# Optimization experiments

Measured on AMD Instinct MI355X. Metric: run time of the kernel, lower is better.

## Reference

```python
import jax, jax.numpy as jnp
import numpy as np

IN_DIM = 512
HID = 1024
E = 16
TOPK = 2


def setup_inputs() -> dict:
    key = jax.random.key(0)
    ks = jax.random.split(key, 8)
    s = 0.02
    x = jax.random.normal(ks[0], (4, 2048, IN_DIM), dtype=jnp.float32)
    Wr = jax.random.normal(ks[1], (IN_DIM, E), dtype=jnp.float32) * s
    br = jnp.zeros((E,), dtype=jnp.float32)
    W1 = jax.random.normal(ks[2], (E, IN_DIM, HID), dtype=jnp.float32) * s
    b1 = jnp.zeros((E, HID), dtype=jnp.float32)
    W2 = jax.random.normal(ks[3], (E, HID, IN_DIM), dtype=jnp.float32) * s
    b2 = jnp.zeros((E, IN_DIM), dtype=jnp.float32)
    return {"x": x, "Wr": Wr, "br": br, "W1": W1, "b1": b1, "W2": W2, "b2": b2}


def reference(x, Wr, br, W1, b1, W2, b2):
    token_shape = x.shape[:-1]
    xf = x.reshape(-1, x.shape[-1])            # [T, D]
    T = xf.shape[0]

    # router (temperature = 1.0)
    logits = xf @ Wr + br                       # [T, E]
    probs = jax.nn.softmax(logits, axis=-1)
    topk_w, topk_idx = jax.lax.top_k(probs, TOPK)           # [T, K]
    topk_w = topk_w / jnp.maximum(topk_w.sum(-1, keepdims=True), 1e-9)

    # combine weights: [T, E], zero where not routed
    combine = jnp.zeros((T, E), dtype=xf.dtype).at[
        jnp.arange(T)[:, None], topk_idx].add(topk_w)

    # per-expert MLP (exact GELU, as torch nn.GELU default), weighted combine
    y = jnp.zeros_like(xf)
    for e in range(E):
        h = jax.nn.gelu(xf @ W1[e] + b1[e], approximate=False)  # [T, H]
        o = h @ W2[e] + b2[e]                                   # [T, D]
        y = y + combine[:, e:e + 1] * o

    # residual (in_dim == out_dim)
    y = xf + y
    return y.reshape(*token_shape, IN_DIM)
```

## Files before the change

kernel.cpp:

```cpp
#include <hip/hip_runtime.h>
#include <hip/hip_bf16.h>
#include <math.h>

#define IN_DIM 512
#define HID    1024
#define NE     16
#define T_TOK  8192
#define NPAIR  (T_TOK*2)

typedef __attribute__((ext_vector_type(8))) short bf16x8;
typedef __attribute__((ext_vector_type(8))) unsigned short ushort8;
typedef __attribute__((ext_vector_type(4))) float f32x4;

__device__ __forceinline__ unsigned short f2b(float f){
  unsigned u = __float_as_uint(f);
  u += 0x7FFF + ((u >> 16) & 1);
  return (unsigned short)(u >> 16);
}
__device__ __forceinline__ float b2f(unsigned short u){
  return __uint_as_float(((unsigned)u) << 16);
}

__device__ __forceinline__ void barrier_lds_only(){
  asm volatile("s_waitcnt lgkmcnt(0)" ::: "memory");
  __builtin_amdgcn_s_barrier();
}

__global__ __launch_bounds__(256) void fused_head(
    const float* __restrict__ x, const float* __restrict__ Wr, const float* __restrict__ br,
    unsigned short* __restrict__ xb, int* __restrict__ eid, float* __restrict__ pw,
    const float* __restrict__ W1, unsigned short* __restrict__ O1,
    const float* __restrict__ W2, unsigned short* __restrict__ O2)
{
  __shared__ float tile[64][65];
  const int b = blockIdx.x;
  const int tid = threadIdx.x;

  if (b < 2048){
    int wid = tid >> 6, lane = tid & 63;
    int t = b*4 + wid;
    const float4* xr4 = (const float4*)(x + (size_t)t*IN_DIM);
    ushort4*      xb4 = (ushort4*)(xb + (size_t)t*IN_DIM);

    float acc[NE];
    #pragma unroll
    for (int i=0;i<NE;i++) acc[i]=0.f;

    #pragma unroll
    for (int j=0;j<2;j++){
      int f = j*64 + lane;
      float4 v = xr4[f];
      ushort4 o; o.x=f2b(v.x); o.y=f2b(v.y); o.z=f2b(v.z); o.w=f2b(v.w);
      xb4[f] = o;
      const float4* wr4 = (const float4*)(Wr + (size_t)(f*4)*NE);
      const float* vv = (const float*)&v;
      #pragma unroll
      for (int rr=0; rr<4; rr++){
        float xv = vv[rr];
        #pragma unroll
        for (int q=0;q<4;q++){
          float4 w = wr4[rr*4+q];
          acc[q*4+0] += xv*w.x; acc[q*4+1] += xv*w.y;
          acc[q*4+2] += xv*w.z; acc[q*4+3] += xv*w.w;
        }
      }
    }
    #pragma unroll
    for (int off=32; off>=1; off>>=1){
      #pragma unroll
      for (int i=0;i<NE;i++) acc[i] += __shfl_xor(acc[i], off, 64);
    }
    if (lane==0){
      #pragma unroll
      for (int i=0;i<NE;i++) acc[i] += br[i];
      int e0=0; float l0=acc[0];
      #pragma unroll
      for (int i=1;i<NE;i++) if (acc[i] > l0){ l0=acc[i]; e0=i; }
      int e1=-1; float l1=-3.0e38f;
      #pragma unroll
      for (int i=0;i<NE;i++) if (i!=e0 && acc[i] > l1){ l1=acc[i]; e1=i; }
      float w0 = 1.f/(1.f + __expf(l1 - l0));
      float w1 = 1.f - w0;
      pw[t*2+0] = w0; pw[t*2+1] = w1;
      eid[t*2+0] = e0; eid[t*2+1] = e1;
    }
    return;
  }

  const float* src; unsigned short* dst; int M, N, m0, n0;
  const int bb = b - 2048;
  if (bb < 2048){
    M = IN_DIM; N = HID;
    int e = bb >> 7, r = bb & 127;
    n0 = (r & 15)*64; m0 = (r >> 4)*64;
    src = W1 + (size_t)e*M*N; dst = O1 + (size_t)e*M*N;
  } else {
    int b2 = bb - 2048; M = HID; N = IN_DIM;
    int e = b2 >> 7, r = b2 & 127;
    n0 = (r & 7)*64; m0 = (r >> 3)*64;
    src = W2 + (size_t)e*M*N; dst = O2 + (size_t)e*M*N;
  }
  const int lr = tid >> 4, lc = (tid & 15)*4;
  #pragma unroll
  for (int i=0;i<4;i++)
    *(float4*)&tile[lr + i*16][lc] = *(const float4*)&src[(size_t)(m0 + lr + i*16)*N + n0 + lc];
  __syncthreads();
  const int nr = tid >> 3, mc = (tid & 7)*8;
  #pragma unroll
  for (int p=0;p<2;p++){
    int n = nr + p*32;
    ushort8 o;
    #pragma unroll
    for (int j=0;j<8;j++) o[j] = f2b(tile[mc+j][n]);
    *(ushort8*)&dst[(size_t)(n0 + n)*M + m0 + mc] = o;
  }
}

__global__ __launch_bounds__(1024) void bucket_kernel(const int* __restrict__ eid,
                                                      int* __restrict__ cnt,
                                                      int* __restrict__ bucket){
  int e = blockIdx.x;
  __shared__ int lbase;
  if (threadIdx.x == 0) lbase = 0;
  __syncthreads();
  int lane = threadIdx.x & 63, wid = threadIdx.x >> 6;
  int* be = bucket + e*T_TOK;
  for (int c = wid*64; c < NPAIR; c += 1024){
    int p = c + lane;
    bool ok = (eid[p] == e);
    unsigned long long m = __ballot(ok);
    int rank = __popcll(m & ((1ull << lane) - 1ull));
    int count = __popcll(m);
    int base = 0;
    if (lane == 0) base = atomicAdd(&lbase, count);
    base = __shfl(base, 0, 64);
    if (ok) be[base + rank] = p;
  }
  __syncthreads();
  if (threadIdx.x == 0) cnt[e] = lbase;
}

template<int KDIM, int NDIM, bool FIRST>
__global__ __launch_bounds__(256) void moe_gemm(
    const unsigned short* __restrict__ A,
    const unsigned short* __restrict__ Bm,
    const float* __restrict__ bias,
    const int* __restrict__ cnt,
    const int* __restrict__ bucket,
    const float* __restrict__ pw,
    unsigned short* __restrict__ hb,
    unsigned short* __restrict__ opb)
{
  constexpr int NS  = KDIM / 32;
  constexpr int NBT = NDIM / 128;

  int ntiles = 0;
  #pragma unroll
  for (int j=0;j<NE;j++) ntiles += ((cnt[j]+63)>>6)*NBT;

  __shared__ unsigned short As[2*64*32];
  __shared__ unsigned short Bs[2*128*32];

  int tid = threadIdx.x;
  int lane = tid & 63, wid = tid >> 6;
  int wm = (wid>>1)*32, wn = (wid&1)*64;
  int lr0 = tid >> 2;
  int c   = tid & 3;
  int sc  = (c ^ ((lr0 >> 1) & 3)) * 8;
  int wA  = lr0*32 + sc;
  int fr = lane & 15, fb = lane >> 4;
  int pf8 = (fb ^ ((fr >> 1) & 3)) * 8;
  int fq = (lane>>4)*4;

  const int t0 = (blockIdx.x & 7)*(gridDim.x >> 3) + (blockIdx.x >> 3);
  for (int t = t0; t < ntiles; t += gridDim.x){
    int e=0, tloc=0, ebase=0, ce=0, itl=1;
    {
      int cum=0, crow=0;
      #pragma unroll
      for (int j=0;j<NE;j++){
        int cj = cnt[j];
        int it = (cj+63)>>6;
        int tj = it * NBT;
        bool in = (t >= cum) & (t < cum+tj);
        if (in){ e=j; tloc=t-cum; ebase=crow; ce=cj; itl=it; }
        cum += tj; crow += cj;
      }
    }
    int i0 = (tloc % itl) * 64;
    int n0 = (tloc / itl) * 128;

    const int* buck = bucket + e*T_TOK;
    int posA = i0 + lr0;
    int arow;
    if (FIRST){
      int pair = (posA < ce) ? buck[posA] : buck[i0];
      arow = pair >> 1;
    } else {
      arow = ebase + posA;
      if (arow > NPAIR-1) arow = NPAIR-1;
    }
    const unsigned short* Ag = A + (size_t)arow*KDIM + c*8;
    const unsigned short* Bg = Bm + (size_t)e*NDIM*KDIM + (size_t)(n0 + lr0)*KDIM + c*8;

    f32x4 acc[2][4];
    #pragma unroll
    for (int a=0;a<2;a++)
      #pragma unroll
      for (int b2=0;b2<4;b2++)
        #pragma unroll
        for (int j=0;j<4;j++) acc[a][b2][j] = 0.f;

    float4 ar, br0, br1;
    ar  = *(const float4*)(Ag);
    br0 = *(const float4*)(Bg);
    br1 = *(const float4*)(Bg + (size_t)64*KDIM);
    *(float4*)(As + wA) = ar;
    *(float4*)(Bs + wA) = br0;
    *(float4*)(Bs + wA + 64*32) = br1;
    ar  = *(const float4*)(Ag + 32);
    br0 = *(const float4*)(Bg + 32);
    br1 = *(const float4*)(Bg + (size_t)64*KDIM + 32);
    barrier_lds_only();

    #pragma unroll 2
    for (int k = 0; k < NS; k++){
      const int cur = k & 1, nxt = cur ^ 1;
      float4 na, nb0, nb1;
      bool ld = (k + 2 < NS);
      if (ld){
        na  = *(const float4*)(Ag + (k+2)*32);
        nb0 = *(const float4*)(Bg + (k+2)*32);
        nb1 = *(const float4*)(Bg + (size_t)64*KDIM + (k+2)*32);
      }
      if (k + 1 < NS){
        *(float4*)(As + nxt*2048 + wA) = ar;
        *(float4*)(Bs + nxt*4096 + wA) = br0;
        *(float4*)(Bs + nxt*4096 + wA + 64*32) = br1;
      }
      if (ld){ ar = na; br0 = nb0; br1 = nb1; }

      const unsigned short* Ac = As + cur*2048;
      const unsigned short* Bc = Bs + cur*4096;
      bf16x8 af[2], bfr[4];
      #pragma unroll
      for (int s=0;s<2;s++) af[s]  = *(const bf16x8*)(Ac + (wm + s*16 + fr)*32 + pf8);
      #pragma unroll
      for (int u=0;u<4;u++) bfr[u] = *(const bf16x8*)(Bc + (wn + u*16 + fr)*32 + pf8);
      #pragma unroll
      for (int s=0;s<2;s++)
        #pragma unroll
        for (int u=0;u<4;u++)
          acc[s][u] = __builtin_amdgcn_mfma_f32_16x16x32_bf16(af[s], bfr[u], acc[s][u], 0,0,0);
      barrier_lds_only();
    }

    #pragma unroll
    for (int s=0;s<2;s++){
      #pragma unroll
      for (int i=0;i<4;i++){
        int row = wm + s*16 + fq + i;
        int pos = i0 + row;
        if (pos >= ce) continue;
        #pragma unroll
        for (int u=0;u<4;u++){
          int n = n0 + wn + u*16 + fr;
          float v = acc[s][u][i] + bias[e*NDIM + n];
          if (FIRST){
            float z2 = v*(1.5957691216057308f + 0.0713548162726009f*v*v);
            float g  = __fdividef(v, 1.f + __expf(-z2));
            hb[(size_t)(ebase + pos)*NDIM + n] = f2b(g);
          } else {
            int pair = buck[pos];
            opb[(size_t)pair*NDIM + n] = f2b(pw[pair]*v);
          }
        }
      }
    }
  }
}

__global__ __launch_bounds__(256) void combine_kernel(const float* __restrict__ x,
                                                      const unsigned short* __restrict__ opb,
                                                      float* __restrict__ out){
  int i = blockIdx.x*256 + threadIdx.x;
  int t  = i >> 7;
  int c4 = i & 127;
  float4 v = ((const float4*)x)[i];
  ushort4 a = ((const ushort4*)opb)[(size_t)(2*t)*128 + c4];
  ushort4 b = ((const ushort4*)opb)[(size_t)(2*t+1)*128 + c4];
  v.x += b2f(a.x) + b2f(b.x);
  v.y += b2f(a.y) + b2f(b.y);
  v.z += b2f(a.z) + b2f(b.z);
  v.w += b2f(a.w) + b2f(b.w);
  ((float4*)out)[i] = v;
}

extern "C" void kernel_launch(void* const* d_in, const int* in_sizes, int n_in,
                              void* d_out, int out_size, void* d_ws, size_t ws_size,
                              hipStream_t stream)
{
  const float* x  = (const float*)d_in[0];
  const float* Wr = (const float*)d_in[1];
  const float* br = (const float*)d_in[2];
  const float* W1 = (const float*)d_in[3];
  const float* b1 = (const float*)d_in[4];
  const float* W2 = (const float*)d_in[5];
  const float* b2 = (const float*)d_in[6];
  float* out = (float*)d_out;
  char* ws = (char*)d_ws;

  int*            cnt    = (int*)(ws + 0);
  int*            bucket = (int*)(ws + 1024);
  float*          pw     = (float*)(ws + 525312);
  unsigned short* xb     = (unsigned short*)(ws + 590848);
  unsigned short* w1t    = (unsigned short*)(ws + 8979456);
  unsigned short* w2t    = (unsigned short*)(ws + 25756672);
  unsigned short* hb     = (unsigned short*)(ws + 42533888);
  int*            eid    = (int*)(ws + 42533888);
  unsigned short* opb    = w1t;

  fused_head<<<6144, 256, 0, stream>>>(x, Wr, br, xb, eid, pw, W1, w1t, W2, w2t);
  bucket_kernel<<<NE, 1024, 0, stream>>>(eid, cnt, bucket);
  moe_gemm<IN_DIM, HID, true ><<<2176, 256, 0, stream>>>(
      xb, w1t, b1, cnt, bucket, pw, hb, opb);
  moe_gemm<HID, IN_DIM, false><<<1088, 256, 0, stream>>>(
      hb, w2t, b2, cnt, bucket, pw, hb, opb);
  combine_kernel<<<(T_TOK*IN_DIM/4)/256, 256, 0, stream>>>(x, opb, out);
}
```

Baseline: 252.3 us.

## Fuse combine into second expert GEMM via atomic adds into output

The residual x is written to the output in the head kernel, and the second expert GEMM atomically adds weighted fp32 expert outputs directly into the output. The separate combine kernel and the bf16 intermediate buffer go away, which removes one launch and a full read/write pass. In exchange there are 8M scattered fp32 atomic adds, and the summation order becomes non-deterministic.

```diff
diff --git a/kernel.cpp b/kernel.cpp
--- a/kernel.cpp
+++ b/kernel.cpp
@@ -30,7 +30,8 @@
     const float* __restrict__ x, const float* __restrict__ Wr, const float* __restrict__ br,
     unsigned short* __restrict__ xb, int* __restrict__ eid, float* __restrict__ pw,
     const float* __restrict__ W1, unsigned short* __restrict__ O1,
-    const float* __restrict__ W2, unsigned short* __restrict__ O2)
+    const float* __restrict__ W2, unsigned short* __restrict__ O2,
+    float* __restrict__ out)
 {
   __shared__ float tile[64][65];
   const int b = blockIdx.x;
@@ -41,6 +42,7 @@
     int t = b*4 + wid;
     const float4* xr4 = (const float4*)(x + (size_t)t*IN_DIM);
     ushort4*      xb4 = (ushort4*)(xb + (size_t)t*IN_DIM);
+    float4*       ot4 = (float4*)(out + (size_t)t*IN_DIM);
 
     float acc[NE];
     #pragma unroll
@@ -52,6 +54,7 @@
       float4 v = xr4[f];
       ushort4 o; o.x=f2b(v.x); o.y=f2b(v.y); o.z=f2b(v.z); o.w=f2b(v.w);
       xb4[f] = o;
+      ot4[f] = v;
       const float4* wr4 = (const float4*)(Wr + (size_t)(f*4)*NE);
       const float* vv = (const float*)&v;
       #pragma unroll
@@ -149,7 +152,7 @@
     const int* __restrict__ bucket,
     const float* __restrict__ pw,
     unsigned short* __restrict__ hb,
-    unsigned short* __restrict__ opb)
+    float* __restrict__ out)
 {
   constexpr int NS  = KDIM / 32;
   constexpr int NBT = NDIM / 128;
@@ -272,28 +275,12 @@
             hb[(size_t)(ebase + pos)*NDIM + n] = f2b(g);
           } else {
             int pair = buck[pos];
-            opb[(size_t)pair*NDIM + n] = f2b(pw[pair]*v);
+            atomicAdd(&out[(size_t)(pair >> 1)*NDIM + n], pw[pair]*v);
           }
         }
       }
     }
   }
-}
-
-__global__ __launch_bounds__(256) void combine_kernel(const float* __restrict__ x,
-                                                      const unsigned short* __restrict__ opb,
-                                                      float* __restrict__ out){
-  int i = blockIdx.x*256 + threadIdx.x;
-  int t  = i >> 7;
-  int c4 = i & 127;
-  float4 v = ((const float4*)x)[i];
-  ushort4 a = ((const ushort4*)opb)[(size_t)(2*t)*128 + c4];
-  ushort4 b = ((const ushort4*)opb)[(size_t)(2*t+1)*128 + c4];
-  v.x += b2f(a.x) + b2f(b.x);
-  v.y += b2f(a.y) + b2f(b.y);
-  v.z += b2f(a.z) + b2f(b.z);
-  v.w += b2f(a.w) + b2f(b.w);
-  ((float4*)out)[i] = v;
 }
 
 extern "C" void kernel_launch(void* const* d_in, const int* in_sizes, int n_in,
@@ -318,13 +305,11 @@
   unsigned short* w2t    = (unsigned short*)(ws + 25756672);
   unsigned short* hb     = (unsigned short*)(ws + 42533888);
   int*            eid    = (int*)(ws + 42533888);
-  unsigned short* opb    = w1t;
-
-  fused_head<<<6144, 256, 0, stream>>>(x, Wr, br, xb, eid, pw, W1, w1t, W2, w2t);
+
+  fused_head<<<6144, 256, 0, stream>>>(x, Wr, br, xb, eid, pw, W1, w1t, W2, w2t, out);
   bucket_kernel<<<NE, 1024, 0, stream>>>(eid, cnt, bucket);
   moe_gemm<IN_DIM, HID, true ><<<2176, 256, 0, stream>>>(
-      xb, w1t, b1, cnt, bucket, pw, hb, opb);
+      xb, w1t, b1, cnt, bucket, pw, hb, out);
   moe_gemm<HID, IN_DIM, false><<<1088, 256, 0, stream>>>(
-      hb, w2t, b2, cnt, bucket, pw, hb, opb);
-  combine_kernel<<<(T_TOK*IN_DIM/4)/256, 256, 0, stream>>>(x, opb, out);
-}
+      hb, w2t, b2, cnt, bucket, pw, hb, out);
+}
```

Measured after the change: 271.4 us. 1.08x slower.

## Fuse expert bucketing into MoE GEMM blocks and drop separate bucket kernel

Applied to the files above, without the earlier changes.

Removes the standalone bucket kernel, which ran on only 16 blocks, along with its global count and bucket arrays. Each GEMM block instead counts expert assignments by ballot over the full eid array. For every tile it then scans eid again, builds per-chunk prefix sums in shared memory and gathers only its own 64 row indices into LDS. This saves one launch and a poorly parallel serial stage. The cost is redundant scanning of all 16K routing entries in every block, plus extra barriers per tile. The eid buffer is moved so it no longer aliases the hidden activations.

```diff
diff --git a/kernel.cpp b/kernel.cpp
--- a/kernel.cpp
+++ b/kernel.cpp
@@ -116,54 +116,54 @@
   }
 }
 
-__global__ __launch_bounds__(1024) void bucket_kernel(const int* __restrict__ eid,
-                                                      int* __restrict__ cnt,
-                                                      int* __restrict__ bucket){
-  int e = blockIdx.x;
-  __shared__ int lbase;
-  if (threadIdx.x == 0) lbase = 0;
-  __syncthreads();
-  int lane = threadIdx.x & 63, wid = threadIdx.x >> 6;
-  int* be = bucket + e*T_TOK;
-  for (int c = wid*64; c < NPAIR; c += 1024){
-    int p = c + lane;
-    bool ok = (eid[p] == e);
-    unsigned long long m = __ballot(ok);
-    int rank = __popcll(m & ((1ull << lane) - 1ull));
-    int count = __popcll(m);
-    int base = 0;
-    if (lane == 0) base = atomicAdd(&lbase, count);
-    base = __shfl(base, 0, 64);
-    if (ok) be[base + rank] = p;
-  }
-  __syncthreads();
-  if (threadIdx.x == 0) cnt[e] = lbase;
-}
-
 template<int KDIM, int NDIM, bool FIRST>
 __global__ __launch_bounds__(256) void moe_gemm(
     const unsigned short* __restrict__ A,
     const unsigned short* __restrict__ Bm,
     const float* __restrict__ bias,
-    const int* __restrict__ cnt,
-    const int* __restrict__ bucket,
+    const int* __restrict__ eid,
     const float* __restrict__ pw,
     unsigned short* __restrict__ hb,
     unsigned short* __restrict__ opb)
 {
   constexpr int NS  = KDIM / 32;
   constexpr int NBT = NDIM / 128;
+  constexpr int NCH = NPAIR / 64;
+
+  __shared__ unsigned short As[2*64*32];
+  __shared__ unsigned short Bs[2*128*32];
+  __shared__ int cnt_sm[NE];
+  __shared__ int wpart[4][NE];
+  __shared__ int chunkpre[NCH];
+  __shared__ int lbuck[64];
+
+  int tid = threadIdx.x;
+  int lane = tid & 63, wv = tid >> 6;
+
+  {
+    int pc[NE];
+    #pragma unroll
+    for (int e2=0;e2<NE;e2++) pc[e2]=0;
+    for (int c2 = wv; c2 < NCH; c2 += 4){
+      int v = eid[c2*64 + lane];
+      #pragma unroll
+      for (int e2=0;e2<NE;e2++)
+        pc[e2] += __popcll(__ballot(v==e2));
+    }
+    if (lane==0){
+      #pragma unroll
+      for (int e2=0;e2<NE;e2++) wpart[wv][e2]=pc[e2];
+    }
+    __syncthreads();
+    if (tid < NE) cnt_sm[tid] = wpart[0][tid]+wpart[1][tid]+wpart[2][tid]+wpart[3][tid];
+    __syncthreads();
+  }
 
   int ntiles = 0;
   #pragma unroll
-  for (int j=0;j<NE;j++) ntiles += ((cnt[j]+63)>>6)*NBT;
-
-  __shared__ unsigned short As[2*64*32];
-  __shared__ unsigned short Bs[2*128*32];
-
-  int tid = threadIdx.x;
-  int lane = tid & 63, wid = tid >> 6;
-  int wm = (wid>>1)*32, wn = (wid&1)*64;
+  for (int j=0;j<NE;j++) ntiles += ((cnt_sm[j]+63)>>6)*NBT;
+
+  int wm = (wv>>1)*32, wn = (wv&1)*64;
   int lr0 = tid >> 2;
   int c   = tid & 3;
   int sc  = (c ^ ((lr0 >> 1) & 3)) * 8;
@@ -179,7 +179,7 @@
       int cum=0, crow=0;
       #pragma unroll
       for (int j=0;j<NE;j++){
-        int cj = cnt[j];
+        int cj = cnt_sm[j];
         int it = (cj+63)>>6;
         int tj = it * NBT;
         bool in = (t >= cum) & (t < cum+tj);
@@ -190,12 +190,44 @@
     int i0 = (tloc % itl) * 64;
     int n0 = (tloc / itl) * 128;
 
-    const int* buck = bucket + e*T_TOK;
+    __syncthreads();
+    for (int c2 = wv; c2 < NCH; c2 += 4){
+      unsigned long long m = __ballot(eid[c2*64 + lane] == e);
+      if (lane==0) chunkpre[c2] = __popcll(m);
+    }
+    if (tid < 64) lbuck[tid] = -1;
+    __syncthreads();
+    if (wv==0){
+      int vals[4];
+      #pragma unroll
+      for (int j=0;j<4;j++) vals[j] = chunkpre[lane*4+j];
+      int lsum = vals[0]+vals[1]+vals[2]+vals[3];
+      int pre = lsum;
+      #pragma unroll
+      for (int off=1; off<64; off<<=1){
+        int o = __shfl_up(pre, off, 64);
+        if (lane>=off) pre += o;
+      }
+      pre -= lsum;
+      #pragma unroll
+      for (int j=0;j<4;j++){ chunkpre[lane*4+j] = pre; pre += vals[j]; }
+    }
+    __syncthreads();
+    for (int c2 = wv; c2 < NCH; c2 += 4){
+      int p = c2*64 + lane;
+      bool ok = (eid[p] == e);
+      unsigned long long m = __ballot(ok);
+      int rank = chunkpre[c2] + __popcll(m & ((1ull << lane) - 1ull));
+      if (ok && rank >= i0 && rank < i0+64) lbuck[rank - i0] = p;
+    }
+    __syncthreads();
+    if (tid < 64 && lbuck[tid] < 0) lbuck[tid] = lbuck[0];
+    __syncthreads();
+
     int posA = i0 + lr0;
     int arow;
     if (FIRST){
-      int pair = (posA < ce) ? buck[posA] : buck[i0];
-      arow = pair >> 1;
+      arow = lbuck[lr0] >> 1;
     } else {
       arow = ebase + posA;
       if (arow > NPAIR-1) arow = NPAIR-1;
@@ -271,7 +303,7 @@
             float g  = __fdividef(v, 1.f + __expf(-z2));
             hb[(size_t)(ebase + pos)*NDIM + n] = f2b(g);
           } else {
-            int pair = buck[pos];
+            int pair = lbuck[row];
             opb[(size_t)pair*NDIM + n] = f2b(pw[pair]*v);
           }
         }
@@ -310,21 +342,18 @@
   float* out = (float*)d_out;
   char* ws = (char*)d_ws;
 
-  int*            cnt    = (int*)(ws + 0);
-  int*            bucket = (int*)(ws + 1024);
+  int*            eid    = (int*)(ws + 1024);
   float*          pw     = (float*)(ws + 525312);
   unsigned short* xb     = (unsigned short*)(ws + 590848);
   unsigned short* w1t    = (unsigned short*)(ws + 8979456);
   unsigned short* w2t    = (unsigned short*)(ws + 25756672);
   unsigned short* hb     = (unsigned short*)(ws + 42533888);
-  int*            eid    = (int*)(ws + 42533888);
   unsigned short* opb    = w1t;
 
   fused_head<<<6144, 256, 0, stream>>>(x, Wr, br, xb, eid, pw, W1, w1t, W2, w2t);
-  bucket_kernel<<<NE, 1024, 0, stream>>>(eid, cnt, bucket);
   moe_gemm<IN_DIM, HID, true ><<<2176, 256, 0, stream>>>(
-      xb, w1t, b1, cnt, bucket, pw, hb, opb);
+      xb, w1t, b1, eid, pw, hb, opb);
   moe_gemm<HID, IN_DIM, false><<<1088, 256, 0, stream>>>(
-      hb, w2t, b2, cnt, bucket, pw, hb, opb);
+      hb, w2t, b2, eid, pw, hb, opb);
   combine_kernel<<<(T_TOK*IN_DIM/4)/256, 256, 0, stream>>>(x, opb, out);
 }
```

Result: slower. 421.7 us (+67.1%).
